# Kernel optimization log

Hardware: AMD Instinct MI355X
Metric: run time of the kernel (lower is better)

## Reference

```python
import jax, jax.numpy as jnp
import numpy as np

B = 262144
INPUT_DIM = 512
HID = 64
NUM_BASE = 2
NUM_CLASSES = 2


def setup_inputs() -> dict:
    key = jax.random.key(0)
    ks = jax.random.split(key, 10)
    probs = jax.random.uniform(ks[0], (B, NUM_BASE, NUM_CLASSES), dtype=jnp.float32)
    fuzzy_features = jax.random.normal(ks[1], (B, INPUT_DIM), dtype=jnp.float32)
    s1 = 1.0 / np.sqrt(INPUT_DIM)
    s2 = 1.0 / np.sqrt(HID)
    # m1: Linear(input_dim,64) -> ReLU -> Linear(64, num_base*num_classes)
    W1 = jax.random.uniform(ks[2], (INPUT_DIM, HID), jnp.float32, -s1, s1)
    b1 = jax.random.uniform(ks[3], (HID,), jnp.float32, -s1, s1)
    W2 = jax.random.uniform(ks[4], (HID, NUM_BASE * NUM_CLASSES), jnp.float32, -s2, s2)
    b2 = jax.random.uniform(ks[5], (NUM_BASE * NUM_CLASSES,), jnp.float32, -s2, s2)
    # m2: Linear(input_dim,64) -> ReLU -> Linear(64, num_classes)
    W3 = jax.random.uniform(ks[6], (INPUT_DIM, HID), jnp.float32, -s1, s1)
    b3 = jax.random.uniform(ks[7], (HID,), jnp.float32, -s1, s1)
    W4 = jax.random.uniform(ks[8], (HID, NUM_CLASSES), jnp.float32, -s2, s2)
    b4 = jax.random.uniform(ks[9], (NUM_CLASSES,), jnp.float32, -s2, s2)
    return {"probs": probs, "fuzzy_features": fuzzy_features,
            "W1": W1, "b1": b1, "W2": W2, "b2": b2,
            "W3": W3, "b3": b3, "W4": W4, "b4": b4}


def _forward(probs, x, W1, b1, W2, b2, W3, b3, W4, b4):
    # FuzzyMeasureLearner
    h1 = jax.nn.relu(x @ W1 + b1)                       # [B, 64]
    single = jax.nn.sigmoid((h1 @ W2 + b2).reshape(-1, NUM_BASE, NUM_CLASSES))
    h2 = jax.nn.relu(x @ W3 + b3)                       # [B, 64]
    inc = jax.nn.sigmoid(h2 @ W4 + b4)                  # [B, 2]
    # Vectorized Choquet integral (binary, 2 sources)
    p0 = probs[:, 0, :]                                 # [B, 2]
    p1 = probs[:, 1, :]
    mu1 = single[:, 0, :]
    mu2 = single[:, 1, :]
    mu12 = jnp.minimum(jnp.maximum(mu1, mu2) + inc, 1.0)
    res = jnp.where(p0 <= p1,
                    p0 * mu1 + (p1 - p0) * mu12,
                    p1 * mu2 + (p0 - p1) * mu12)        # [B, 2]
    return jax.nn.softmax(res, axis=1)


def reference(probs, fuzzy_features, W1, b1, W2, b2, W3, b3, W4, b4):
    return _forward(probs, fuzzy_features, W1, b1, W2, b2, W3, b3, W4, b4)
```

## Files before the change

### kernel.cpp

```cpp
#include <hip/hip_runtime.h>
#include <hip/hip_bf16.h>

typedef short s16x8 __attribute__((ext_vector_type(8)));
typedef unsigned u32x4 __attribute__((ext_vector_type(4)));
typedef float f32x4 __attribute__((ext_vector_type(4)));
typedef float f32x2 __attribute__((ext_vector_type(2)));

static __device__ __forceinline__ short f2bf(float f) {
    unsigned u = __builtin_bit_cast(unsigned, f);
    unsigned r = (u + 0x7fffu + ((u >> 16) & 1u)) >> 16;
    return (short)r;
}

static __device__ __forceinline__ unsigned pk2bf(float a, float b) {
    __hip_bfloat162 h = __float22bfloat162_rn(make_float2(a, b));
    unsigned r;
    __builtin_memcpy(&r, &h, sizeof(r));
    return r;
}

__global__ void prep_weights(const float* __restrict__ W1,
                             const float* __restrict__ W3,
                             short* __restrict__ bws) {
    int tid = blockIdx.x * blockDim.x + threadIdx.x;
    int j  = tid & 7;
    int l  = (tid >> 3) & 63;
    int nt = (tid >> 9) & 7;
    int kk = tid >> 12;
    int k = kk * 32 + ((l >> 4) << 3) + j;
    int n = nt * 16 + (l & 15);
    float v = (n < 64) ? W1[k * 64 + n] : W3[k * 64 + (n - 64)];
    bws[tid] = f2bf(v);
}

__global__ __launch_bounds__(1024, 4)
void mf2_main(const float* __restrict__ probs, const float* __restrict__ x,
              const short* __restrict__ bws,
              const float* __restrict__ b1, const float* __restrict__ W2,
              const float* __restrict__ b2, const float* __restrict__ b3,
              const float* __restrict__ W4, const float* __restrict__ b4,
              float* __restrict__ out)
{
    __shared__ short bsh[512 * 128];

    const int tid  = threadIdx.x;
    const int lane = tid & 63;
    const int wv   = tid >> 6;
    const int g    = lane >> 4;
    const int m    = lane & 15;
    const long rowBase = (long)blockIdx.x * 256 + wv * 16;

    const float* xp = x + (rowBase + m) * 512 + g * 8;

    f32x4 ra[4][2];
    #pragma unroll
    for (int p = 0; p < 4; ++p) {
        const float* pp = xp + p * 32;
        ra[p][0] = *(const f32x4*)pp;
        ra[p][1] = *(const f32x4*)(pp + 4);
    }

    {
        const f32x4* src = (const f32x4*)bws;
        f32x4* dst = (f32x4*)bsh;
        #pragma unroll
        for (int it = 0; it < 8; ++it) {
            const int idx = it * 1024 + tid;
            dst[idx] = src[idx];
        }
    }
    __syncthreads();

    const s16x8* bls = (const s16x8*)bsh + lane;

    f32x4 acc[8];
    #pragma unroll
    for (int nt = 0; nt < 8; ++nt)
        acc[nt] = (f32x4){0.f, 0.f, 0.f, 0.f};

    #pragma unroll
    for (int kk = 0; kk < 16; ++kk) {
        const int s = kk & 3;
        u32x4 pa;
        pa[0] = pk2bf(ra[s][0][0], ra[s][0][1]);
        pa[1] = pk2bf(ra[s][0][2], ra[s][0][3]);
        pa[2] = pk2bf(ra[s][1][0], ra[s][1][1]);
        pa[3] = pk2bf(ra[s][1][2], ra[s][1][3]);
        s16x8 a = __builtin_bit_cast(s16x8, pa);

        if (kk < 12) {
            const float* pp = xp + (kk + 4) * 32;
            ra[s][0] = *(const f32x4*)pp;
            ra[s][1] = *(const f32x4*)(pp + 4);
        }

        #pragma unroll
        for (int nt = 0; nt < 8; ++nt) {
            s16x8 b = bls[kk * 512 + nt * 64];
            acc[nt] = __builtin_amdgcn_mfma_f32_16x16x32_bf16(a, b, acc[nt], 0, 0, 0);
        }
    }

    float w2r[4][4];
    float w4r[4][2];
    float biasr[8];
    #pragma unroll
    for (int nt = 0; nt < 4; ++nt) {
        const int col = m + 16 * nt;
        f32x4 w2v = *(const f32x4*)(W2 + col * 4);
        #pragma unroll
        for (int c = 0; c < 4; ++c) w2r[nt][c] = w2v[c];
        f32x2 w4v = *(const f32x2*)(W4 + col * 2);
        w4r[nt][0] = w4v[0]; w4r[nt][1] = w4v[1];
    }
    #pragma unroll
    for (int nt = 0; nt < 8; ++nt) {
        const int col = m + 16 * nt;
        biasr[nt] = (col < 64) ? b1[col] : b3[col - 64];
    }
    float b2v[4], b4v[2];
    #pragma unroll
    for (int c = 0; c < 4; ++c) b2v[c] = b2[c];
    #pragma unroll
    for (int c = 0; c < 2; ++c) b4v[c] = b4[c];

    float own[6] = {0.f, 0.f, 0.f, 0.f, 0.f, 0.f};
    #pragma unroll
    for (int r = 0; r < 4; ++r) {
        float v[6] = {0.f, 0.f, 0.f, 0.f, 0.f, 0.f};
        #pragma unroll
        for (int nt = 0; nt < 4; ++nt) {
            float h = fmaxf(acc[nt][r] + biasr[nt], 0.f);
            v[0] += h * w2r[nt][0];
            v[1] += h * w2r[nt][1];
            v[2] += h * w2r[nt][2];
            v[3] += h * w2r[nt][3];
        }
        #pragma unroll
        for (int j = 0; j < 4; ++j) {
            float h = fmaxf(acc[4 + j][r] + biasr[4 + j], 0.f);
            v[4] += h * w4r[j][0];
            v[5] += h * w4r[j][1];
        }
        #pragma unroll
        for (int msk = 1; msk <= 8; msk <<= 1) {
            #pragma unroll
            for (int c = 0; c < 6; ++c) v[c] += __shfl_xor(v[c], msk, 64);
        }
        if (m == r) {
            #pragma unroll
            for (int c = 0; c < 6; ++c) own[c] = v[c];
        }
    }

    if (m < 4) {
        const long row = rowBase + g * 4 + m;
        f32x4 pr = *(const f32x4*)(probs + row * 4);
        float mu1[2], mu2[2], icv[2];
        #pragma unroll
        for (int c = 0; c < 2; ++c) {
            mu1[c] = 1.0f / (1.0f + __expf(-(own[c]     + b2v[c])));
            mu2[c] = 1.0f / (1.0f + __expf(-(own[2 + c] + b2v[2 + c])));
            icv[c] = 1.0f / (1.0f + __expf(-(own[4 + c] + b4v[c])));
        }
        float res[2];
        #pragma unroll
        for (int c = 0; c < 2; ++c) {
            float p0 = pr[c], p1 = pr[2 + c];
            float m12 = fminf(fmaxf(mu1[c], mu2[c]) + icv[c], 1.0f);
            res[c] = (p0 <= p1) ? (p0 * mu1[c] + (p1 - p0) * m12)
                                : (p1 * mu2[c] + (p0 - p1) * m12);
        }
        float d01 = res[0] - res[1];
        f32x2 o;
        o[0] = 1.0f / (1.0f + __expf(-d01));
        o[1] = 1.0f / (1.0f + __expf(d01));
        *(f32x2*)(out + row * 2) = o;
    }
}

extern "C" void kernel_launch(void* const* d_in, const int* in_sizes, int n_in,
                              void* d_out, int out_size, void* d_ws, size_t ws_size,
                              hipStream_t stream)
{
    const float* probs = (const float*)d_in[0];
    const float* x     = (const float*)d_in[1];
    const float* W1    = (const float*)d_in[2];
    const float* b1    = (const float*)d_in[3];
    const float* W2    = (const float*)d_in[4];
    const float* b2    = (const float*)d_in[5];
    const float* W3    = (const float*)d_in[6];
    const float* b3    = (const float*)d_in[7];
    const float* W4    = (const float*)d_in[8];
    const float* b4    = (const float*)d_in[9];
    float* out = (float*)d_out;
    short* bws = (short*)d_ws;

    hipLaunchKernelGGL(prep_weights, dim3(256), dim3(256), 0, stream, W1, W3, bws);
    hipLaunchKernelGGL(mf2_main, dim3(1024), dim3(1024), 0, stream,
                       probs, x, bws, b1, W2, b2, b3, W4, b4, out);
}
```

Before: 127.1 us.

## Remap K dimension so each lane loads contiguous 128-byte chunks of x

Permutes the K-index assignment in the bf16 weight prep so each 16-lane group owns a contiguous 32-float run of every 128-element slice of x. The main kernel then issues eight consecutive 16-byte loads per lane per chunk, replacing the earlier pattern of 32-byte pieces strided across the row, and double-buffers the chunks across the four outer iterations. The aim is better global-load coalescing and fewer memory transactions. The cost is higher register pressure from the 2x8 float4 buffer, which could hurt occupancy at 1024 threads per block.

```diff
diff --git a/kernel.cpp b/kernel.cpp
--- a/kernel.cpp
+++ b/kernel.cpp
@@ -27,7 +27,8 @@
     int l  = (tid >> 3) & 63;
     int nt = (tid >> 9) & 7;
     int kk = tid >> 12;
-    int k = kk * 32 + ((l >> 4) << 3) + j;
+    int g  = l >> 4;
+    int k = ((kk >> 2) << 7) + (g << 5) + ((kk & 3) << 3) + j;
     int n = nt * 16 + (l & 15);
     float v = (n < 64) ? W1[k * 64 + n] : W3[k * 64 + (n - 64)];
     bws[tid] = f2bf(v);
@@ -50,15 +51,12 @@
     const int m    = lane & 15;
     const long rowBase = (long)blockIdx.x * 256 + wv * 16;
 
-    const float* xp = x + (rowBase + m) * 512 + g * 8;
-
-    f32x4 ra[4][2];
-    #pragma unroll
-    for (int p = 0; p < 4; ++p) {
-        const float* pp = xp + p * 32;
-        ra[p][0] = *(const f32x4*)pp;
-        ra[p][1] = *(const f32x4*)(pp + 4);
-    }
+    const float* xp = x + (rowBase + m) * 512 + g * 32;
+
+    f32x4 ra[2][8];
+    #pragma unroll
+    for (int q = 0; q < 8; ++q)
+        ra[0][q] = *((const f32x4*)xp + q);
 
     {
         const f32x4* src = (const f32x4*)bws;
@@ -79,25 +77,32 @@
         acc[nt] = (f32x4){0.f, 0.f, 0.f, 0.f};
 
     #pragma unroll
-    for (int kk = 0; kk < 16; ++kk) {
-        const int s = kk & 3;
-        u32x4 pa;
-        pa[0] = pk2bf(ra[s][0][0], ra[s][0][1]);
-        pa[1] = pk2bf(ra[s][0][2], ra[s][0][3]);
-        pa[2] = pk2bf(ra[s][1][0], ra[s][1][1]);
-        pa[3] = pk2bf(ra[s][1][2], ra[s][1][3]);
-        s16x8 a = __builtin_bit_cast(s16x8, pa);
-
-        if (kk < 12) {
-            const float* pp = xp + (kk + 4) * 32;
-            ra[s][0] = *(const f32x4*)pp;
-            ra[s][1] = *(const f32x4*)(pp + 4);
-        }
-
-        #pragma unroll
-        for (int nt = 0; nt < 8; ++nt) {
-            s16x8 b = bls[kk * 512 + nt * 64];
-            acc[nt] = __builtin_amdgcn_mfma_f32_16x16x32_bf16(a, b, acc[nt], 0, 0, 0);
+    for (int c = 0; c < 4; ++c) {
+        s16x8 a[4];
+        #pragma unroll
+        for (int s = 0; s < 4; ++s) {
+            u32x4 pa;
+            pa[0] = pk2bf(ra[c & 1][2 * s][0],     ra[c & 1][2 * s][1]);
+            pa[1] = pk2bf(ra[c & 1][2 * s][2],     ra[c & 1][2 * s][3]);
+            pa[2] = pk2bf(ra[c & 1][2 * s + 1][0], ra[c & 1][2 * s + 1][1]);
+            pa[3] = pk2bf(ra[c & 1][2 * s + 1][2], ra[c & 1][2 * s + 1][3]);
+            a[s] = __builtin_bit_cast(s16x8, pa);
+        }
+
+        if (c < 3) {
+            #pragma unroll
+            for (int q = 0; q < 8; ++q)
+                ra[(c + 1) & 1][q] = *((const f32x4*)(xp + (c + 1) * 128) + q);
+        }
+
+        #pragma unroll
+        for (int s = 0; s < 4; ++s) {
+            const int kk = c * 4 + s;
+            #pragma unroll
+            for (int nt = 0; nt < 8; ++nt) {
+                s16x8 b = bls[kk * 512 + nt * 64];
+                acc[nt] = __builtin_amdgcn_mfma_f32_16x16x32_bf16(a[s], b, acc[nt], 0, 0, 0);
+            }
         }
     }
 
```

New measurement: 161.9 us. 27.4% more time.

## Stage X tiles through swizzled LDS with coalesced row loads and split-K halves

Applied to the files above, without the earlier changes.

Each wave now loads its 16 rows of x with fully coalesced row-contiguous float4 loads, converts them to bf16, and writes them into a new XOR-swizzled LDS buffer. The MFMA operands are then read back from LDS instead of the strided per-lane global loads used before. The K dimension is processed in two halves, with the B weights reloaded into a half-size LDS buffer between them and the second x half prefetched into registers during the first half's MFMAs. Blocks shrink to 512 threads and the grid doubles. The cost is extra LDS traffic and barriers, plus higher register pressure from holding 16 float4 values per lane.

```diff
diff --git a/kernel.cpp b/kernel.cpp
--- a/kernel.cpp
+++ b/kernel.cpp
@@ -3,6 +3,7 @@
 
 typedef short s16x8 __attribute__((ext_vector_type(8)));
 typedef unsigned u32x4 __attribute__((ext_vector_type(4)));
+typedef unsigned u32x2 __attribute__((ext_vector_type(2)));
 typedef float f32x4 __attribute__((ext_vector_type(4)));
 typedef float f32x2 __attribute__((ext_vector_type(2)));
 
@@ -33,7 +34,7 @@
     bws[tid] = f2bf(v);
 }
 
-__global__ __launch_bounds__(1024, 4)
+__global__ __launch_bounds__(512, 2)
 void mf2_main(const float* __restrict__ probs, const float* __restrict__ x,
               const short* __restrict__ bws,
               const float* __restrict__ b1, const float* __restrict__ W2,
@@ -41,33 +42,41 @@
               const float* __restrict__ W4, const float* __restrict__ b4,
               float* __restrict__ out)
 {
-    __shared__ short bsh[512 * 128];
+    __shared__ short bsh[256 * 128];
+    __shared__ short ash[128 * 256];
 
     const int tid  = threadIdx.x;
     const int lane = tid & 63;
-    const int wv   = tid >> 6;
+    const int w    = tid >> 6;
     const int g    = lane >> 4;
     const int m    = lane & 15;
-    const long rowBase = (long)blockIdx.x * 256 + wv * 16;
-
-    const float* xp = x + (rowBase + m) * 512 + g * 8;
-
-    f32x4 ra[4][2];
-    #pragma unroll
-    for (int p = 0; p < 4; ++p) {
-        const float* pp = xp + p * 32;
-        ra[p][0] = *(const f32x4*)pp;
-        ra[p][1] = *(const f32x4*)(pp + 4);
-    }
-
-    {
-        const f32x4* src = (const f32x4*)bws;
-        f32x4* dst = (f32x4*)bsh;
-        #pragma unroll
-        for (int it = 0; it < 8; ++it) {
-            const int idx = it * 1024 + tid;
-            dst[idx] = src[idx];
-        }
+    const long waveRow = (long)blockIdx.x * 128 + w * 16;
+
+    const float* xw = x + waveRow * 512 + lane * 4;
+
+    const int kkL = lane >> 3, g2 = (lane >> 1) & 3, jh = lane & 1;
+    char* ab = (char*)ash;
+
+    f32x4 ra[16];
+
+    #pragma unroll
+    for (int it = 0; it < 16; ++it)
+        ra[it] = *(const f32x4*)(xw + it * 512);
+
+    const f32x4* bsrc = (const f32x4*)bws;
+    f32x4* bdst = (f32x4*)bsh;
+    #pragma unroll
+    for (int it = 0; it < 8; ++it)
+        bdst[it * 512 + tid] = bsrc[it * 512 + tid];
+
+    #pragma unroll
+    for (int it = 0; it < 16; ++it) {
+        u32x2 v;
+        v[0] = pk2bf(ra[it][0], ra[it][1]);
+        v[1] = pk2bf(ra[it][2], ra[it][3]);
+        int addr = w * 8192 + kkL * 1024 + (g2 * 16 + it) * 16 + jh * 8;
+        addr ^= ((addr >> 10) & 7) << 4;
+        *(u32x2*)(ab + addr) = v;
     }
     __syncthreads();
 
@@ -79,21 +88,41 @@
         acc[nt] = (f32x4){0.f, 0.f, 0.f, 0.f};
 
     #pragma unroll
-    for (int kk = 0; kk < 16; ++kk) {
-        const int s = kk & 3;
-        u32x4 pa;
-        pa[0] = pk2bf(ra[s][0][0], ra[s][0][1]);
-        pa[1] = pk2bf(ra[s][0][2], ra[s][0][3]);
-        pa[2] = pk2bf(ra[s][1][0], ra[s][1][1]);
-        pa[3] = pk2bf(ra[s][1][2], ra[s][1][3]);
-        s16x8 a = __builtin_bit_cast(s16x8, pa);
-
-        if (kk < 12) {
-            const float* pp = xp + (kk + 4) * 32;
-            ra[s][0] = *(const f32x4*)pp;
-            ra[s][1] = *(const f32x4*)(pp + 4);
-        }
-
+    for (int it = 0; it < 16; ++it)
+        ra[it] = *(const f32x4*)(xw + it * 512 + 256);
+
+    #pragma unroll
+    for (int kk = 0; kk < 8; ++kk) {
+        int aaddr = w * 8192 + kk * 1024 + lane * 16;
+        aaddr ^= ((aaddr >> 10) & 7) << 4;
+        s16x8 a = *(const s16x8*)(ab + aaddr);
+        #pragma unroll
+        for (int nt = 0; nt < 8; ++nt) {
+            s16x8 b = bls[kk * 512 + nt * 64];
+            acc[nt] = __builtin_amdgcn_mfma_f32_16x16x32_bf16(a, b, acc[nt], 0, 0, 0);
+        }
+    }
+    __syncthreads();
+
+    #pragma unroll
+    for (int it = 0; it < 8; ++it)
+        bdst[it * 512 + tid] = bsrc[4096 + it * 512 + tid];
+    #pragma unroll
+    for (int it = 0; it < 16; ++it) {
+        u32x2 v;
+        v[0] = pk2bf(ra[it][0], ra[it][1]);
+        v[1] = pk2bf(ra[it][2], ra[it][3]);
+        int addr = w * 8192 + kkL * 1024 + (g2 * 16 + it) * 16 + jh * 8;
+        addr ^= ((addr >> 10) & 7) << 4;
+        *(u32x2*)(ab + addr) = v;
+    }
+    __syncthreads();
+
+    #pragma unroll
+    for (int kk = 0; kk < 8; ++kk) {
+        int aaddr = w * 8192 + kk * 1024 + lane * 16;
+        aaddr ^= ((aaddr >> 10) & 7) << 4;
+        s16x8 a = *(const s16x8*)(ab + aaddr);
         #pragma unroll
         for (int nt = 0; nt < 8; ++nt) {
             s16x8 b = bls[kk * 512 + nt * 64];
@@ -154,7 +183,7 @@
     }
 
     if (m < 4) {
-        const long row = rowBase + g * 4 + m;
+        const long row = waveRow + g * 4 + m;
         f32x4 pr = *(const f32x4*)(probs + row * 4);
         float mu1[2], mu2[2], icv[2];
         #pragma unroll
@@ -197,6 +226,6 @@
     short* bws = (short*)d_ws;
 
     hipLaunchKernelGGL(prep_weights, dim3(256), dim3(256), 0, stream, W1, W3, bws);
-    hipLaunchKernelGGL(mf2_main, dim3(1024), dim3(1024), 0, stream,
+    hipLaunchKernelGGL(mf2_main, dim3(2048), dim3(512), 0, stream,
                        probs, x, bws, b1, W2, b2, b3, W4, b4, out);
 }
```

New measurement: 143.1 us. 1.13x slower.
